# Kernel optimization log

Hardware: AMD Instinct MI355X
Metric: run time of the kernel (lower is better)

Reference implementation:

```python
import jax, jax.numpy as jnp
import numpy as np

RADIUS = 0.2
NSAMPLE = 32


def ball_query(radius, nsample, xyz, new_xyz):
    # xyz: (B, N, 3), new_xyz: (B, M, 3) -> idx: (B, M, nsample) int32
    N = xyz.shape[1]
    # squared distances (B, M, N)
    d2 = jnp.sum((new_xyz[:, :, None, :] - xyz[:, None, :, :]) ** 2, axis=-1)
    # key = point index if within radius else N (sentinel); take nsample smallest keys
    key = jnp.where(d2 < radius * radius, jnp.arange(N, dtype=jnp.int32), N)
    neg_top, _ = jax.lax.top_k(-key, nsample)  # ascending keys = earliest in-radius indices
    idx = -neg_top  # (B, M, nsample)
    valid = idx < N
    first = idx[..., :1]
    first = jnp.where(first < N, first, 0)  # if ball empty, fall back to index 0
    return jnp.where(valid, idx, first)


def group_points(features, idx):
    # features: (B, C, N), idx: (B, M, S) -> (B, C, M, S)
    return jax.vmap(lambda f, i: f[:, i])(features, idx)


def setup_inputs() -> dict:
    key = jax.random.key(0)
    k1, k2, k3 = jax.random.split(key, 3)
    B, N, M, C = 4, 16384, 2048, 64
    xyz = jax.random.uniform(k1, (B, N, 3), dtype=jnp.float32)
    new_xyz = jax.random.uniform(k2, (B, M, 3), dtype=jnp.float32)
    features = jax.random.normal(k3, (B, C, N), dtype=jnp.float32)
    return {"xyz": xyz, "new_xyz": new_xyz, "features": features}


def reference(xyz, new_xyz, features):
    idx = ball_query(RADIUS, NSAMPLE, xyz, new_xyz)  # (B, M, S)
    xyz_t = jnp.transpose(xyz, (0, 2, 1))  # (B, 3, N)
    grouped_xyz = group_points(xyz_t, idx)  # (B, 3, M, S)
    grouped_xyz = grouped_xyz - jnp.transpose(new_xyz, (0, 2, 1))[..., None]
    grouped_features = group_points(features, idx)  # (B, C, M, S)
    # use_xyz=True: concat relative coordinates with grouped features
    return jnp.concatenate([grouped_xyz, grouped_features], axis=1)  # (B, 3+C, M, S)
```

## Files before the change

### kernel.cpp

```cpp
#include <hip/hip_runtime.h>


typedef float vf4 __attribute__((ext_vector_type(4)));

#define WPB 2
constexpr int Bc = 4, Nc = 16384, Mc = 2048, Cc = 64, Sc = 32;
constexpr int NQ = Bc * Mc;

__global__ __launch_bounds__(256) void prep_kernel(
    const float* __restrict__ feat,
    const float* __restrict__ xyz,
    float* __restrict__ featT,
    vf4* __restrict__ xyz4)
{
    const int i   = blockIdx.x;
    const int xcd = i & 7;
    const int b   = xcd >> 1;

    if (i >= 1024) {
        const int j    = (i - 1024) >> 3;
        const int idxb = ((xcd & 1) << 5) + j;
        const int t    = idxb * 256 + threadIdx.x;
        const float* p = xyz + ((size_t)b * Nc + t) * 3;
        vf4 v; v.x = p[0]; v.y = p[1]; v.z = p[2]; v.w = 0.0f;
        xyz4[(size_t)b * Nc + t] = v;
        return;
    }

    __shared__ float tile[64][65];
    const int nbase = ((((xcd & 1) << 7) + (i >> 3)) << 6);
    const int tn = threadIdx.x & 63;
    const int tq = threadIdx.x >> 6;
    const float* fb = feat + (size_t)b * Cc * Nc;
    float* ob = featT + (size_t)b * Nc * Cc;
    #pragma unroll
    for (int k = 0; k < 16; ++k) {
        const int c = k * 4 + tq;
        tile[tn][c] = fb[(size_t)c * Nc + nbase + tn];
    }
    __syncthreads();
    #pragma unroll
    for (int k = 0; k < 16; ++k) {
        const int nl = k * 4 + tq;
        ob[(size_t)(nbase + nl) * Cc + tn] = tile[nl][tn];
    }
}

__global__ __launch_bounds__(128) void qg_kernel(
    const vf4* __restrict__ xyz4,
    const float* __restrict__ new_xyz,
    const float* __restrict__ featT,
    float* __restrict__ out)
{
#pragma clang fp contract(off)
    const int lane = threadIdx.x & 63;
    const int wv   = threadIdx.x >> 6;

    const int xcd = blockIdx.x & 7;
    const int b   = xcd >> 1;
    const int m   = ((xcd & 1) << 10) + (blockIdx.x >> 3) * WPB + wv;

    __shared__ int sidx[WPB][Sc];

    const float r2 = 0.2f * 0.2f;
    const float* nz = new_xyz + (size_t)(b * Mc + m) * 3;
    const float qx = nz[0], qy = nz[1], qz = nz[2];
    const vf4* xb4 = xyz4 + (size_t)b * Nc;

    int count = 0, firstIdx = 0;
    const unsigned long long lt = (1ull << lane) - 1ull;

    vf4 pv[4];
    #pragma unroll
    for (int u = 0; u < 4; ++u) pv[u] = xb4[u * 64 + lane];
    for (int base = 0; base < Nc; base += 256) {
        const int nb = (base + 256 < Nc) ? base + 256 : base;
        vf4 nv[4];
        #pragma unroll
        for (int u = 0; u < 4; ++u) nv[u] = xb4[nb + u * 64 + lane];
        #pragma unroll
        for (int u = 0; u < 4; ++u) {
            const float dx = qx - pv[u].x, dy = qy - pv[u].y, dz = qz - pv[u].z;
            float d2 = dx * dx + dy * dy;
            d2 = d2 + dz * dz;
            const bool in = d2 < r2;
            const unsigned long long mask = __ballot(in);
            if (in) {
                const int slot = count + __popcll(mask & lt);
                if (slot < Sc) sidx[wv][slot] = base + u * 64 + lane;
            }
            if (count == 0 && mask != 0ull)
                firstIdx = base + u * 64 + __builtin_ctzll(mask);
            count += __popcll(mask);
        }
        if (count >= Sc) break;
        #pragma unroll
        for (int u = 0; u < 4; ++u) pv[u] = nv[u];
    }
    {
        const int start = count < Sc ? count : Sc;
        if (start + lane < Sc) sidx[wv][start + lane] = firstIdx;
    }
    asm volatile("s_waitcnt lgkmcnt(0)" ::: "memory");

    float* ob = out + ((size_t)b * 67 * Mc + m) * Sc;

    {
        const int s     = lane & 31;
        const int chalf = lane >> 5;
        const int myid  = sidx[wv][s];
        const vf4 p = xb4[myid];
        if (chalf == 0) {
            __builtin_nontemporal_store(p.x - qx, &ob[(size_t)0 * (Mc * Sc) + s]);
            __builtin_nontemporal_store(p.z - qz, &ob[(size_t)2 * (Mc * Sc) + s]);
        } else {
            __builtin_nontemporal_store(p.y - qy, &ob[(size_t)1 * (Mc * Sc) + s]);
        }
    }

    const int cqlo = lane & 7;
    const int sq   = lane >> 3;
    int id4[4];
    #pragma unroll
    for (int k = 0; k < 4; ++k) id4[k] = sidx[wv][4 * sq + k];
    const float* fbase = featT + (size_t)b * Nc * Cc;

    #pragma unroll
    for (int i = 0; i < 2; ++i) {
        const int cq = cqlo + 8 * i;
        vf4 v[4];
        #pragma unroll
        for (int k = 0; k < 4; ++k)
            v[k] = *(const vf4*)(fbase + (size_t)id4[k] * Cc + 4 * cq);
        #pragma unroll
        for (int j = 0; j < 4; ++j) {
            vf4 w;
            w.x = v[0][j]; w.y = v[1][j]; w.z = v[2][j]; w.w = v[3][j];
            __builtin_nontemporal_store(
                w, (vf4*)&ob[(size_t)(3 + 4 * cq + j) * (Mc * Sc) + 4 * sq]);
        }
    }
}

__global__ __launch_bounds__(256) void qg_fallback_kernel(
    const float* __restrict__ xyz, const float* __restrict__ new_xyz,
    const float* __restrict__ feat, float* __restrict__ out)
{
#pragma clang fp contract(off)
    const int lane = threadIdx.x & 63;
    const int wv   = threadIdx.x >> 6;
    const int q    = blockIdx.x * 4 + wv;
    const int b    = q >> 11;
    const int m    = q & (Mc - 1);
    __shared__ int sidx[4][Sc];
    const float r2 = 0.2f * 0.2f;
    const float* nz = new_xyz + (size_t)(b * Mc + m) * 3;
    const float qx = nz[0], qy = nz[1], qz = nz[2];
    const float* xb = xyz + (size_t)b * Nc * 3;
    int count = 0, firstIdx = 0;
    const unsigned long long lt = (1ull << lane) - 1ull;
    for (int base = 0; base < Nc; base += 64) {
        const int i = base + lane;
        const float px = xb[i * 3], py = xb[i * 3 + 1], pz = xb[i * 3 + 2];
        const float dx = qx - px, dy = qy - py, dz = qz - pz;
        float d2 = dx * dx + dy * dy; d2 = d2 + dz * dz;
        const bool in = d2 < r2;
        const unsigned long long mask = __ballot(in);
        if (in) {
            const int slot = count + __popcll(mask & lt);
            if (slot < Sc) sidx[wv][slot] = i;
        }
        if (count == 0 && mask != 0ull) firstIdx = base + __builtin_ctzll(mask);
        count += __popcll(mask);
        if (count >= Sc) break;
    }
    const int start = count < Sc ? count : Sc;
    if (start + lane < Sc) sidx[wv][start + lane] = firstIdx;
    asm volatile("s_waitcnt lgkmcnt(0)" ::: "memory");
    const int s = lane & 31, chalf = lane >> 5;
    const int myid = sidx[wv][s];
    float* ob = out + ((size_t)b * 67 * Mc + m) * Sc;
    ob[(size_t)chalf * (Mc * Sc) + s] = xb[(size_t)myid * 3 + chalf] - (chalf ? qy : qx);
    if (chalf == 0)
        ob[(size_t)2 * (Mc * Sc) + s] = xb[(size_t)myid * 3 + 2] - qz;
    const float* fb = feat + (size_t)b * Cc * Nc;
    #pragma unroll
    for (int it = 0; it < 32; ++it) {
        const int c = it * 2 + chalf;
        ob[(size_t)(3 + c) * (Mc * Sc) + s] = fb[(size_t)c * Nc + myid];
    }
}

extern "C" void kernel_launch(void* const* d_in, const int* in_sizes, int n_in,
                              void* d_out, int out_size, void* d_ws, size_t ws_size,
                              hipStream_t stream) {
    const float* xyz     = (const float*)d_in[0];
    const float* new_xyz = (const float*)d_in[1];
    const float* feat    = (const float*)d_in[2];
    float* out           = (float*)d_out;

    const size_t featT_bytes = (size_t)Bc * Nc * Cc * sizeof(float);
    const size_t xyz4_bytes  = (size_t)Bc * Nc * sizeof(vf4);

    if (ws_size >= featT_bytes + xyz4_bytes) {
        float* featT = (float*)d_ws;
        vf4*   xyz4  = (vf4*)((char*)d_ws + featT_bytes);
        hipLaunchKernelGGL(prep_kernel, dim3(1280), dim3(256), 0, stream,
                           feat, xyz, featT, xyz4);
        hipLaunchKernelGGL(qg_kernel, dim3(NQ / WPB), dim3(128), 0, stream,
                           xyz4, new_xyz, featT, out);
    } else {
        hipLaunchKernelGGL(qg_fallback_kernel, dim3(NQ / 4), dim3(256), 0, stream,
                           xyz, new_xyz, feat, out);
    }
}
```

Baseline: 33.31 us.

## Scan raw xyz with two-deep prefetch instead of padded xyz4 in query loop

The ball-query scan now reads the original packed xyz array (three scalar loads per point) rather than the padded float4 copy, and prefetches two 256-point chunks ahead instead of one. A min-blocks hint of 8 is added to the launch bounds. The intent is to hide global load latency in the early-exit scan and to cut the bytes read per point. In exchange there are more load instructions, strided uncoalesced-looking scalar accesses, and higher register pressure under the tighter occupancy bound.

```diff
diff --git a/kernel.cpp b/kernel.cpp
--- a/kernel.cpp
+++ b/kernel.cpp
@@ -46,7 +46,8 @@
     }
 }
 
-__global__ __launch_bounds__(128) void qg_kernel(
+__global__ __launch_bounds__(128, 8) void qg_kernel(
+    const float* __restrict__ xyz,
     const vf4* __restrict__ xyz4,
     const float* __restrict__ new_xyz,
     const float* __restrict__ featT,
@@ -65,22 +66,33 @@
     const float r2 = 0.2f * 0.2f;
     const float* nz = new_xyz + (size_t)(b * Mc + m) * 3;
     const float qx = nz[0], qy = nz[1], qz = nz[2];
-    const vf4* xb4 = xyz4 + (size_t)b * Nc;
+    const float* xb = xyz + (size_t)b * Nc * 3;
 
     int count = 0, firstIdx = 0;
     const unsigned long long lt = (1ull << lane) - 1ull;
 
-    vf4 pv[4];
-    #pragma unroll
-    for (int u = 0; u < 4; ++u) pv[u] = xb4[u * 64 + lane];
+    float ax[4], ay[4], az[4], bx[4], by[4], bz[4];
+    #pragma unroll
+    for (int u = 0; u < 4; ++u) {
+        const float* pp = xb + (size_t)(u * 64 + lane) * 3;
+        ax[u] = pp[0]; ay[u] = pp[1]; az[u] = pp[2];
+    }
+    #pragma unroll
+    for (int u = 0; u < 4; ++u) {
+        const float* pp = xb + (size_t)(256 + u * 64 + lane) * 3;
+        bx[u] = pp[0]; by[u] = pp[1]; bz[u] = pp[2];
+    }
     for (int base = 0; base < Nc; base += 256) {
-        const int nb = (base + 256 < Nc) ? base + 256 : base;
-        vf4 nv[4];
-        #pragma unroll
-        for (int u = 0; u < 4; ++u) nv[u] = xb4[nb + u * 64 + lane];
+        const int nb2 = (base + 512 < Nc) ? base + 512 : base;
+        float cx[4], cy[4], cz[4];
         #pragma unroll
         for (int u = 0; u < 4; ++u) {
-            const float dx = qx - pv[u].x, dy = qy - pv[u].y, dz = qz - pv[u].z;
+            const float* pp = xb + (size_t)(nb2 + u * 64 + lane) * 3;
+            cx[u] = pp[0]; cy[u] = pp[1]; cz[u] = pp[2];
+        }
+        #pragma unroll
+        for (int u = 0; u < 4; ++u) {
+            const float dx = qx - ax[u], dy = qy - ay[u], dz = qz - az[u];
             float d2 = dx * dx + dy * dy;
             d2 = d2 + dz * dz;
             const bool in = d2 < r2;
@@ -95,7 +107,10 @@
         }
         if (count >= Sc) break;
         #pragma unroll
-        for (int u = 0; u < 4; ++u) pv[u] = nv[u];
+        for (int u = 0; u < 4; ++u) {
+            ax[u] = bx[u]; ay[u] = by[u]; az[u] = bz[u];
+            bx[u] = cx[u]; by[u] = cy[u]; bz[u] = cz[u];
+        }
     }
     {
         const int start = count < Sc ? count : Sc;
@@ -109,7 +124,7 @@
         const int s     = lane & 31;
         const int chalf = lane >> 5;
         const int myid  = sidx[wv][s];
-        const vf4 p = xb4[myid];
+        const vf4 p = xyz4[(size_t)b * Nc + myid];
         if (chalf == 0) {
             __builtin_nontemporal_store(p.x - qx, &ob[(size_t)0 * (Mc * Sc) + s]);
             __builtin_nontemporal_store(p.z - qz, &ob[(size_t)2 * (Mc * Sc) + s]);
@@ -208,7 +223,7 @@
         hipLaunchKernelGGL(prep_kernel, dim3(1280), dim3(256), 0, stream,
                            feat, xyz, featT, xyz4);
         hipLaunchKernelGGL(qg_kernel, dim3(NQ / WPB), dim3(128), 0, stream,
-                           xyz4, new_xyz, featT, out);
+                           xyz, xyz4, new_xyz, featT, out);
     } else {
         hipLaunchKernelGGL(qg_fallback_kernel, dim3(NQ / 4), dim3(256), 0, stream,
                            xyz, new_xyz, feat, out);
```

After: 35.22 us. +5.7%, slower.
